# Performance work log

Measured on AMD Instinct MI355X. Metric: run time of the kernel, lower is better.

The kernel has to match this reference:

```python
import jax, jax.numpy as jnp
import numpy as np

H = 128; B = 128; NA = 32; N = B * NA; NH = 4; DH = H // NH; F = 2 * H + 3


def _ln(x, g, b, eps=1e-5):
    m = x.mean(-1, keepdims=True)
    v = ((x - m) ** 2).mean(-1, keepdims=True)
    return (x - m) / jnp.sqrt(v + eps) * g + b


def _silu(x):
    return x * jax.nn.sigmoid(x)


def setup_inputs() -> dict:
    key = jax.random.key(0)
    ks = jax.random.split(key, 16)
    def rn(i, shape, s=0.05):
        return jax.random.normal(ks[i], shape, jnp.float32) * s
    return dict(
        num_atoms=jnp.full((B,), NA, dtype=jnp.int32),
        elems=jax.random.randint(ks[0], (N,), 0, 119),
        cell=jnp.tile(10.0 * jnp.eye(3, dtype=jnp.float32), (B, 1)),  # [3B,3]
        coord=jax.random.uniform(ks[1], (N, 3), jnp.float32, 1.0, 9.0),
        emb=rn(2, (119, H), 1.0),
        ln_in_g=jnp.ones((H,), jnp.float32), ln_in_b=jnp.zeros((H,), jnp.float32),
        attn_in_w=rn(3, (H, 3 * H)), attn_in_b=jnp.zeros((3 * H,), jnp.float32),
        attn_out_w=rn(4, (H, H)), attn_out_b=jnp.zeros((H,), jnp.float32),
        ce_w1=rn(5, (3, H)), ce_b1=jnp.zeros((H,), jnp.float32),
        ce_w2=rn(6, (H, H)), ce_b2=jnp.zeros((H,), jnp.float32),
        ln_feat_g=jnp.ones((F,), jnp.float32), ln_feat_b=jnp.zeros((F,), jnp.float32),
        op_w1=rn(7, (F, H)), op_b1=jnp.zeros((H,), jnp.float32),
        op_ln1_g=jnp.ones((H,), jnp.float32), op_ln1_b=jnp.zeros((H,), jnp.float32),
        res_w1=rn(8, (H, H)), res_b1=jnp.zeros((H,), jnp.float32),
        res_ln_g=jnp.ones((H,), jnp.float32), res_ln_b=jnp.zeros((H,), jnp.float32),
        res_w2=rn(9, (H, H)), res_b2=jnp.zeros((H,), jnp.float32),
        op_ln2_g=jnp.ones((H,), jnp.float32), op_ln2_b=jnp.zeros((H,), jnp.float32),
        op_w3=rn(10, (H, 3)), op_b3=jnp.zeros((3,), jnp.float32),
    )


def reference(num_atoms, elems, cell, coord, emb, ln_in_g, ln_in_b,
              attn_in_w, attn_in_b, attn_out_w, attn_out_b,
              ce_w1, ce_b1, ce_w2, ce_b2, ln_feat_g, ln_feat_b,
              op_w1, op_b1, op_ln1_g, op_ln1_b,
              res_w1, res_b1, res_ln_g, res_ln_b, res_w2, res_b2,
              op_ln2_g, op_ln2_b, op_w3, op_b3):
    n = coord.shape[0]
    # atom embedding + input LayerNorm
    x = _ln(emb[elems], ln_in_g, ln_in_b)
    # unbatched multihead self-attention over all atoms (seq_len = n)
    qkv = x @ attn_in_w + attn_in_b
    q, k, v = jnp.split(qkv, 3, axis=-1)
    q = q.reshape(n, NH, DH); k = k.reshape(n, NH, DH); v = v.reshape(n, NH, DH)
    a = jax.nn.softmax(jnp.einsum('qhd,khd->hqk', q, k) / np.float32(np.sqrt(DH)), axis=-1)
    x = jnp.einsum('hqk,khd->qhd', a, v).reshape(n, H) @ attn_out_w + attn_out_b
    # cell encoder on [3B,3] rows
    cf = _silu(cell @ ce_w1 + ce_b1) @ ce_w2 + ce_b2
    bidx = jnp.repeat(jnp.arange(num_atoms.shape[0]), num_atoms, total_repeat_length=n)
    # torch: cf.repeat(B,1)[batch_idx] == cf[batch_idx] since batch_idx < B
    comb = _ln(jnp.concatenate([x, cf[bidx], coord], axis=-1), ln_feat_g, ln_feat_b)
    # offset predictor
    h = _silu(_ln(comb @ op_w1 + op_b1, op_ln1_g, op_ln1_b))
    h = h + (_silu(_ln(h @ res_w1 + res_b1, res_ln_g, res_ln_b)) @ res_w2 + res_b2)
    h = _ln(h, op_ln2_g, op_ln2_b)
    offset = jnp.tanh(h @ op_w3 + op_b3) * 0.01
    perturbed = coord + offset
    # per-molecule clamp: segment gather of per-cell-row min/max replaces the python loop
    c3 = cell.reshape(-1, 3, 3)           # [B,3,3]
    cmin = c3.min(axis=2) + 1e-6          # [B,3]
    cmax = c3.max(axis=2) - 1e-6          # [B,3]
    return jnp.clip(perturbed, cmin[bidx], cmax[bidx])
```

## Files before the change

kernel.cpp:

```cpp
#include <hip/hip_runtime.h>
#include <hip/hip_bf16.h>
#include <math.h>
#include <stdint.h>

#define NATOMS 4096
#define HD     128
#define NHEAD  4
#define DHEAD  32
#define FDIM   259
#define BATCH  128
#define H3X    384
#define SPLIT  4

typedef __attribute__((ext_vector_type(8))) short short8;
typedef __attribute__((ext_vector_type(4))) float float4v;
typedef __attribute__((ext_vector_type(16))) float f32x16;

__device__ __forceinline__ ushort f2bf(float f) {
    uint32_t u = __float_as_uint(f);
    return (ushort)((u + 0x7fffu + ((u >> 16) & 1u)) >> 16);
}
__device__ __forceinline__ float b2f(ushort u) {
    return __uint_as_float(((uint32_t)u) << 16);
}
__device__ __forceinline__ f32x16 z16() {
    f32x16 v;
#pragma unroll
    for (int i = 0; i < 16; i++) v[i] = 0.f;
    return v;
}

__global__ __launch_bounds__(256) void k_qkv(const int* __restrict__ elems,
                                             const float* __restrict__ emb,
                                             const float* __restrict__ lg,
                                             const float* __restrict__ lb,
                                             const float* __restrict__ qkvw,
                                             const float* __restrict__ bias,
                                             ushort* __restrict__ Qb, ushort* __restrict__ Kb,
                                             ushort* __restrict__ VTb2) {
    __shared__ alignas(16) ushort Wl[48 * 512];
    __shared__ alignas(16) ushort Af[4][64][8];
    __shared__ alignas(16) ushort vt[128][16];
    const int t = threadIdx.x, w = t >> 6, lane = t & 63, quad = lane >> 4, lq = lane & 15;
    const int rg = blockIdx.x >> 1, half = blockIdx.x & 1;
    const int rb = rg * 16;

#pragma unroll
    for (int m = 0; m < 12; m++) {
        int s = t + 256 * m;
        int chunk = s >> 6, l = s & 63;
        int ntl = chunk >> 2, kt = chunk & 3;
        int q8 = (l >> 4) * 8, lqq = l & 15;
        int n = half * 192 + ntl * 16 + lqq;
        int k0 = kt * 32 + q8;
        ushort o[8];
#pragma unroll
        for (int j = 0; j < 8; j++) o[j] = f2bf(qkvw[(k0 + j) * H3X + n]);
        *(uint4*)&Wl[(chunk << 9) + (l << 3)] = *(uint4*)o;
    }

    {
        int row = t >> 4, seg = t & 15;
        int e = elems[rb + row];
        const float* ep = emb + (size_t)e * HD + seg * 8;
        float v[8]; float s = 0.f, ss = 0.f;
#pragma unroll
        for (int j = 0; j < 8; j++) { v[j] = ep[j]; s += v[j]; ss += v[j] * v[j]; }
#pragma unroll
        for (int m = 1; m < 16; m <<= 1) { s += __shfl_xor(s, m); ss += __shfl_xor(ss, m); }
        float mean = s * (1.f / HD);
        float inv = rsqrtf(ss * (1.f / HD) - mean * mean + 1e-5f);
        ushort o[8];
#pragma unroll
        for (int j = 0; j < 8; j++)
            o[j] = f2bf((v[j] - mean) * inv * lg[seg * 8 + j] + lb[seg * 8 + j]);
        *(uint4*)&Af[seg >> 2][(seg & 3) * 16 + row][0] = *(uint4*)o;
    }
    __syncthreads();

    float4v acc[3];
#pragma unroll
    for (int i = 0; i < 3; i++) acc[i] = (float4v){0.f, 0.f, 0.f, 0.f};
#pragma unroll
    for (int kt = 0; kt < 4; kt++) {
        short8 af = *(const short8*)&Af[kt][lane][0];
#pragma unroll
        for (int i = 0; i < 3; i++) {
            short8 wf = *(const short8*)&Wl[((((w * 3 + i) << 2) + kt) << 9) + (lane << 3)];
            acc[i] = __builtin_amdgcn_mfma_f32_16x16x32_bf16(af, wf, acc[i], 0, 0, 0);
        }
    }
#pragma unroll
    for (int i = 0; i < 3; i++) {
        int col = lq + 16 * (half * 12 + w * 3 + i);
        float bb = bias[col];
#pragma unroll
        for (int r = 0; r < 4; r++) {
            float c = acc[i][r] + bb;
            int rowin = quad * 4 + r;
            int row = rb + rowin;
            if (col < 128) {
                Qb[(size_t)(((col >> 5) * NATOMS) + row) * 32 + (col & 31)] = f2bf(c * 0.25503483f);
            } else if (col < 256) {
                int cc = col - 128;
                Kb[(size_t)(((cc >> 5) * NATOMS) + row) * 32 + (cc & 31)] = f2bf(c);
            } else {
                vt[col - 256][rowin] = f2bf(c);
            }
        }
    }
    __syncthreads();
    if (half == 1 && t < 128) {
        int hh = t >> 5, d = t & 31;
        uint4 a0 = *(const uint4*)&vt[t][0];
        uint4 a1 = *(const uint4*)&vt[t][8];
        ushort* dst = VTb2 + ((size_t)(hh * 64 + (rb >> 6)) * 32 + d) * 64 + (rb & 63);
        *(uint4*)(dst) = a0;
        *(uint4*)(dst + 8) = a1;
    }
}

__global__ __launch_bounds__(256) void k_attn(const ushort* __restrict__ Qb,
                                              const ushort* __restrict__ Kb,
                                              const ushort* __restrict__ VTb2,
                                              ushort* __restrict__ Opart,
                                              float* __restrict__ lpart,
                                              const int* __restrict__ num_atoms,
                                              const float* __restrict__ cell,
                                              const float* __restrict__ aow,
                                              const float* __restrict__ op1w,
                                              const float* __restrict__ r1w,
                                              const float* __restrict__ r2w,
                                              const float* __restrict__ ce_w1,
                                              const float* __restrict__ ce_b1,
                                              const float* __restrict__ ce_w2,
                                              const float* __restrict__ ce_b2,
                                              int* __restrict__ bidx,
                                              float* __restrict__ cmin,
                                              float* __restrict__ cmax,
                                              ushort* __restrict__ Wao,
                                              ushort* __restrict__ Wop1,
                                              ushort* __restrict__ Wr1,
                                              ushort* __restrict__ Wr2,
                                              float* __restrict__ CF) {
    __shared__ alignas(16) ushort P_s[4][32 * 72];
    __shared__ alignas(16) float OL[2][32 * 36];
    __shared__ float LL[2][32];
    const int t = threadIdx.x;

    if (blockIdx.z == SPLIT) {
        float* hs = (float*)&P_s[0][0];
        int* start = (int*)&P_s[1][0];
        const int mid = blockIdx.y * 64 + blockIdx.x;
        for (int j = mid * 256 + t; j < 86016; j += 65536) {
            if (j < 16384) {
                int k = j >> 7, n = j & 127;
                Wao[n * 128 + k] = f2bf(aow[j]);
            } else if (j < 49536) {
                int jj = j - 16384; int k = jj >> 7, n = jj & 127;
                Wop1[n * 288 + k] = f2bf(op1w[jj]);
            } else if (j < 53248) {
                int jj = j - 49536; int n = jj & 127, k = 259 + (jj >> 7);
                Wop1[n * 288 + k] = 0;
            } else if (j < 69632) {
                int jj = j - 53248; int k = jj >> 7, n = jj & 127;
                Wr1[n * 128 + k] = f2bf(r1w[jj]);
            } else {
                int jj = j - 69632; int k = jj >> 7, n = jj & 127;
                Wr2[n * 128 + k] = f2bf(r2w[jj]);
            }
        }
        if (mid < 128) {
            if (t < 128) {
                float c0 = cell[mid * 3 + 0], c1 = cell[mid * 3 + 1], c2 = cell[mid * 3 + 2];
                float h = c0 * ce_w1[t] + c1 * ce_w1[HD + t] + c2 * ce_w1[2 * HD + t] + ce_b1[t];
                h = h / (1.f + __expf(-h));
                hs[t] = h;
            }
            __syncthreads();
            if (t < 128) {
                float acc = ce_b2[t];
#pragma unroll 8
                for (int k = 0; k < HD; k++) acc += hs[k] * ce_w2[k * HD + t];
                CF[mid * HD + t] = acc;
            }
        } else if (mid == 128) {
            if (t == 0) {
                int pos = 0;
                for (int b = 0; b < BATCH; b++) { start[b] = pos; pos += num_atoms[b]; }
                start[BATCH] = pos;
            }
            __syncthreads();
            if (t < 128) {
                int s = min(start[t], NATOMS), e = min(start[t + 1], NATOMS);
                for (int j = s; j < e; j++) bidx[j] = t;
                if (t == 0) {
                    int total = min(start[BATCH], NATOMS);
                    for (int j = total; j < NATOMS; j++) bidx[j] = BATCH - 1;
                }
            }
            for (int rr = t; rr < BATCH * 3; rr += 256) {
                float a0 = cell[rr * 3 + 0], a1 = cell[rr * 3 + 1], a2 = cell[rr * 3 + 2];
                cmin[rr] = fminf(a0, fminf(a1, a2)) + 1e-6f;
                cmax[rr] = fmaxf(a0, fmaxf(a1, a2)) - 1e-6f;
            }
        }
        return;
    }

    const int w = t >> 6, lane = t & 63;
    const int l31 = lane & 31, hi = lane >> 5;
    const int qt = w & 1, kh2 = w >> 1;
    const int h = blockIdx.y, sp = blockIdx.z;
    const int q0 = blockIdx.x * 64;
    const int qrow = q0 + qt * 32 + l31;

    short8 qf0 = *(const short8*)(Qb + (size_t)(h * NATOMS + qrow) * 32 + hi * 8);
    short8 qf1 = *(const short8*)(Qb + (size_t)(h * NATOMS + qrow) * 32 + 16 + hi * 8);
    f32x16 O = z16();
    float lp = 0.f;
    ushort* Pw = &P_s[w][0];
    const int kstart = sp * (NATOMS / SPLIT) + kh2 * 64;

    for (int ck = 0; ck < (NATOMS / SPLIT) / 128; ck++) {
        int kb = kstart + ck * 128;
        const ushort* vbase = VTb2 + ((size_t)(h * 64 + (kb >> 6)) * 32 + l31) * 64;
#pragma unroll
        for (int kt = 0; kt < 2; kt++) {
            int kk = kb + kt * 32;
            const ushort* kp = Kb + (size_t)(h * NATOMS + kk + l31) * 32 + hi * 8;
            short8 kf0 = *(const short8*)(kp);
            short8 kf1 = *(const short8*)(kp + 16);
            f32x16 S = z16();
            __builtin_amdgcn_s_setprio(1);
            S = __builtin_amdgcn_mfma_f32_32x32x16_bf16(kf0, qf0, S, 0, 0, 0);
            S = __builtin_amdgcn_mfma_f32_32x32x16_bf16(kf1, qf1, S, 0, 0, 0);
            __builtin_amdgcn_s_setprio(0);
#pragma unroll
            for (int c = 0; c < 4; c++) {
                float p0 = exp2f(S[4 * c + 0]);
                float p1 = exp2f(S[4 * c + 1]);
                float p2 = exp2f(S[4 * c + 2]);
                float p3 = exp2f(S[4 * c + 3]);
                lp += (p0 + p1) + (p2 + p3);
                uint2 u;
                asm("v_cvt_pk_bf16_f32 %0, %1, %2" : "=v"(u.x) : "v"(p0), "v"(p1));
                asm("v_cvt_pk_bf16_f32 %0, %1, %2" : "=v"(u.y) : "v"(p2), "v"(p3));
                *(uint2*)(&Pw[l31 * 72 + kt * 32 + c * 8 + hi * 4]) = u;
            }
#pragma unroll
            for (int wd = 0; wd < 2; wd++) {
                int koff = kt * 32 + wd * 16;
                short8 vf = *(const short8*)(vbase + koff + hi * 8);
                short8 pf = *(const short8*)(&Pw[l31 * 72 + koff + hi * 8]);
                __builtin_amdgcn_s_setprio(1);
                O = __builtin_amdgcn_mfma_f32_32x32x16_bf16(vf, pf, O, 0, 0, 0);
                __builtin_amdgcn_s_setprio(0);
            }
        }
    }
    lp += __shfl_xor(lp, 32);
    if (kh2 == 0) {
#pragma unroll
        for (int c = 0; c < 4; c++) {
            float4 f = {O[4 * c + 0], O[4 * c + 1], O[4 * c + 2], O[4 * c + 3]};
            *(float4*)(&OL[qt][l31 * 36 + c * 8 + hi * 4]) = f;
        }
        if (hi == 0) LL[qt][l31] = lp;
    }
    __syncthreads();
    if (kh2 == 1) {
        lp += LL[qt][l31];
#pragma unroll
        for (int c = 0; c < 4; c++) {
            float4 f = *(const float4*)(&OL[qt][l31 * 36 + c * 8 + hi * 4]);
            float o0 = O[4 * c + 0] + f.x, o1 = O[4 * c + 1] + f.y;
            float o2 = O[4 * c + 2] + f.z, o3 = O[4 * c + 3] + f.w;
            uint2 u;
            u.x = (uint32_t)f2bf(o0) | ((uint32_t)f2bf(o1) << 16);
            u.y = (uint32_t)f2bf(o2) | ((uint32_t)f2bf(o3) << 16);
            *(uint2*)(Opart + (size_t)(sp * NATOMS + qrow) * HD + h * 32 + c * 8 + hi * 4) = u;
        }
        if (hi == 0) lpart[sp * (NHEAD * NATOMS) + h * NATOMS + qrow] = lp;
    }
}

__global__ __launch_bounds__(512) void k_back(
        const ushort* __restrict__ Opart, const float* __restrict__ lpart,
        const ushort* __restrict__ Wao, const float* __restrict__ aob,
        const float* __restrict__ CF, const float* __restrict__ coord,
        const int* __restrict__ bidx,
        const float* __restrict__ fg, const float* __restrict__ fb,
        const ushort* __restrict__ Wop1, const float* __restrict__ op1b,
        const float* __restrict__ l1g, const float* __restrict__ l1b,
        const ushort* __restrict__ Wr1, const float* __restrict__ r1b,
        const float* __restrict__ rlg, const float* __restrict__ rlb,
        const ushort* __restrict__ Wr2, const float* __restrict__ r2b,
        const float* __restrict__ l2g, const float* __restrict__ l2b,
        const float* __restrict__ w3, const float* __restrict__ b3,
        const float* __restrict__ cmin, const float* __restrict__ cmax,
        float* __restrict__ out) {
    __shared__ alignas(16) ushort AF1[9][64][8];
    __shared__ alignas(16) ushort AF2[4][64][8];
    __shared__ alignas(16) ushort AF3[4][64][8];
    __shared__ float RED[8][16][4];
    __shared__ float REDC[16][2];
    __shared__ float COORDS[16][3];
    const int t = threadIdx.x, w = t >> 6, lane = t & 63, quad = lane >> 4, lq = lane & 15;
    const int rb = blockIdx.x * 16;
    const int col = lq + 16 * w;

    const int arow = rb + lq;
    float4v a0 = {0.f, 0.f, 0.f, 0.f};
#pragma unroll
    for (int h = 0; h < 4; h++) {
        float l = 0.f;
#pragma unroll
        for (int s = 0; s < SPLIT; s++) l += lpart[s * (NHEAD * NATOMS) + h * NATOMS + arow];
        float inv = 1.f / l;
        float pv[8];
#pragma unroll
        for (int j = 0; j < 8; j++) pv[j] = 0.f;
#pragma unroll
        for (int s = 0; s < SPLIT; s++) {
            short8 ov = *(const short8*)(Opart + (size_t)(s * NATOMS + arow) * HD + h * 32 + quad * 8);
#pragma unroll
            for (int j = 0; j < 8; j++) pv[j] += b2f((ushort)ov[j]);
        }
        short8 af;
#pragma unroll
        for (int j = 0; j < 8; j++) af[j] = (short)f2bf(pv[j] * inv);
        short8 w0 = *(const short8*)(Wao + (size_t)col * HD + h * 32 + quad * 8);
        a0 = __builtin_amdgcn_mfma_f32_16x16x32_bf16(af, w0, a0, 0, 0, 0);
    }
    float x1[4];
#pragma unroll
    for (int r = 0; r < 4; r++) x1[r] = a0[r] + aob[col];

    float cfv[4];
#pragma unroll
    for (int r = 0; r < 4; r++) cfv[r] = CF[bidx[rb + quad * 4 + r] * HD + col];
#pragma unroll
    for (int r = 0; r < 4; r++) {
        float s1 = x1[r] + cfv[r];
        float s2 = x1[r] * x1[r] + cfv[r] * cfv[r];
#pragma unroll
        for (int m = 1; m < 16; m <<= 1) { s1 += __shfl_xor(s1, m); s2 += __shfl_xor(s2, m); }
        if (lq == 0) { RED[w][quad * 4 + r][0] = s1; RED[w][quad * 4 + r][1] = s2; }
    }
    if (t < 16) {
        float c0 = coord[(rb + t) * 3 + 0], c1 = coord[(rb + t) * 3 + 1], c2 = coord[(rb + t) * 3 + 2];
        COORDS[t][0] = c0; COORDS[t][1] = c1; COORDS[t][2] = c2;
        REDC[t][0] = c0 + c1 + c2; REDC[t][1] = c0 * c0 + c1 * c1 + c2 * c2;
    }
    if (t < 64) { uint4 z = {0, 0, 0, 0}; *(uint4*)&AF1[8][t][0] = z; }
    __syncthreads();
#pragma unroll
    for (int r = 0; r < 4; r++) {
        int ri = quad * 4 + r;
        float s1 = REDC[ri][0], s2 = REDC[ri][1];
#pragma unroll
        for (int ww = 0; ww < 8; ww++) { s1 += RED[ww][ri][0]; s2 += RED[ww][ri][1]; }
        float mn = s1 * (1.f / FDIM);
        float iv = rsqrtf(s2 * (1.f / FDIM) - mn * mn + 1e-5f);
        float vx = (x1[r] - mn) * iv * fg[col] + fb[col];
        float vc = (cfv[r] - mn) * iv * fg[col + 128] + fb[col + 128];
        AF1[col >> 5][((col >> 3) & 3) * 16 + ri][col & 7] = f2bf(vx);
        int c2 = col + 128;
        AF1[c2 >> 5][((c2 >> 3) & 3) * 16 + ri][c2 & 7] = f2bf(vc);
    }
    if (t < 16) {
        float s1 = REDC[t][0], s2 = REDC[t][1];
#pragma unroll
        for (int ww = 0; ww < 8; ww++) { s1 += RED[ww][t][0]; s2 += RED[ww][t][1]; }
        float mn = s1 * (1.f / FDIM);
        float iv = rsqrtf(s2 * (1.f / FDIM) - mn * mn + 1e-5f);
#pragma unroll
        for (int c = 0; c < 3; c++)
            AF1[8][t][c] = f2bf((COORDS[t][c] - mn) * iv * fg[256 + c] + fb[256 + c]);
    }
    __syncthreads();

    float4v cv = {0.f, 0.f, 0.f, 0.f};
#pragma unroll
    for (int kt = 0; kt < 9; kt++) {
        short8 af = *(const short8*)&AF1[kt][lane][0];
        short8 w0 = *(const short8*)(Wop1 + (size_t)col * 288 + kt * 32 + quad * 8);
        cv = __builtin_amdgcn_mfma_f32_16x16x32_bf16(af, w0, cv, 0, 0, 0);
    }
    float h0[4];
#pragma unroll
    for (int r = 0; r < 4; r++) {
        h0[r] = cv[r] + op1b[col];
        float s1 = h0[r], s2 = h0[r] * h0[r];
#pragma unroll
        for (int m = 1; m < 16; m <<= 1) { s1 += __shfl_xor(s1, m); s2 += __shfl_xor(s2, m); }
        if (lq == 0) { RED[w][quad * 4 + r][0] = s1; RED[w][quad * 4 + r][1] = s2; }
    }
    __syncthreads();
#pragma unroll
    for (int r = 0; r < 4; r++) {
        int ri = quad * 4 + r;
        float s1 = 0.f, s2 = 0.f;
#pragma unroll
        for (int ww = 0; ww < 8; ww++) { s1 += RED[ww][ri][0]; s2 += RED[ww][ri][1]; }
        float mn = s1 * (1.f / HD);
        float iv = rsqrtf(s2 * (1.f / HD) - mn * mn + 1e-5f);
        float o = (h0[r] - mn) * iv * l1g[col] + l1b[col];
        o = o / (1.f + __expf(-o));
        AF2[col >> 5][((col >> 3) & 3) * 16 + ri][col & 7] = f2bf(o);
    }
    __syncthreads();

    float4v dv = {0.f, 0.f, 0.f, 0.f};
#pragma unroll
    for (int kt = 0; kt < 4; kt++) {
        short8 af = *(const short8*)&AF2[kt][lane][0];
        short8 w0 = *(const short8*)(Wr1 + (size_t)col * HD + kt * 32 + quad * 8);
        dv = __builtin_amdgcn_mfma_f32_16x16x32_bf16(af, w0, dv, 0, 0, 0);
    }
    float e0[4];
#pragma unroll
    for (int r = 0; r < 4; r++) {
        e0[r] = dv[r] + r1b[col];
        float s1 = e0[r], s2 = e0[r] * e0[r];
#pragma unroll
        for (int m = 1; m < 16; m <<= 1) { s1 += __shfl_xor(s1, m); s2 += __shfl_xor(s2, m); }
        if (lq == 0) { RED[w][quad * 4 + r][0] = s1; RED[w][quad * 4 + r][1] = s2; }
    }
    __syncthreads();
#pragma unroll
    for (int r = 0; r < 4; r++) {
        int ri = quad * 4 + r;
        float s1 = 0.f, s2 = 0.f;
#pragma unroll
        for (int ww = 0; ww < 8; ww++) { s1 += RED[ww][ri][0]; s2 += RED[ww][ri][1]; }
        float mn = s1 * (1.f / HD);
        float iv = rsqrtf(s2 * (1.f / HD) - mn * mn + 1e-5f);
        float o = (e0[r] - mn) * iv * rlg[col] + rlb[col];
        o = o / (1.f + __expf(-o));
        AF3[col >> 5][((col >> 3) & 3) * 16 + ri][col & 7] = f2bf(o);
    }
    __syncthreads();

    float4v fv = {0.f, 0.f, 0.f, 0.f};
#pragma unroll
    for (int kt = 0; kt < 4; kt++) {
        short8 af = *(const short8*)&AF3[kt][lane][0];
        short8 w0 = *(const short8*)(Wr2 + (size_t)col * HD + kt * 32 + quad * 8);
        fv = __builtin_amdgcn_mfma_f32_16x16x32_bf16(af, w0, fv, 0, 0, 0);
    }
    float g0r[4];
#pragma unroll
    for (int r = 0; r < 4; r++) {
        int ri = quad * 4 + r;
        float rs = b2f(AF2[col >> 5][((col >> 3) & 3) * 16 + ri][col & 7]);
        g0r[r] = fv[r] + r2b[col] + rs;
        float s1 = g0r[r], s2 = g0r[r] * g0r[r];
#pragma unroll
        for (int m = 1; m < 16; m <<= 1) { s1 += __shfl_xor(s1, m); s2 += __shfl_xor(s2, m); }
        if (lq == 0) { RED[w][ri][0] = s1; RED[w][ri][1] = s2; }
    }
    __syncthreads();
    float tp[4][3];
#pragma unroll
    for (int r = 0; r < 4; r++) {
        int ri = quad * 4 + r;
        float s1 = 0.f, s2 = 0.f;
#pragma unroll
        for (int ww = 0; ww < 8; ww++) { s1 += RED[ww][ri][0]; s2 += RED[ww][ri][1]; }
        float mn = s1 * (1.f / HD);
        float iv = rsqrtf(s2 * (1.f / HD) - mn * mn + 1e-5f);
        float h2 = (g0r[r] - mn) * iv * l2g[col] + l2b[col];
#pragma unroll
        for (int c = 0; c < 3; c++) {
            float v = h2 * w3[col * 3 + c];
#pragma unroll
            for (int m = 1; m < 16; m <<= 1) v += __shfl_xor(v, m);
            tp[r][c] = v;
        }
    }
    __syncthreads();
    if (lq == 0) {
#pragma unroll
        for (int r = 0; r < 4; r++) {
            RED[w][quad * 4 + r][0] = tp[r][0];
            RED[w][quad * 4 + r][1] = tp[r][1];
            RED[w][quad * 4 + r][2] = tp[r][2];
        }
    }
    __syncthreads();
    if (t < 16) {
        int bi = bidx[rb + t];
#pragma unroll
        for (int c = 0; c < 3; c++) {
            float sv = 0.f;
#pragma unroll
            for (int ww = 0; ww < 8; ww++) sv += RED[ww][t][c];
            float off = tanhf(sv + b3[c]) * 0.01f;
            float pert = COORDS[t][c] + off;
            pert = fminf(fmaxf(pert, cmin[bi * 3 + c]), cmax[bi * 3 + c]);
            out[(rb + t) * 3 + c] = pert;
        }
    }
}

extern "C" void kernel_launch(void* const* d_in, const int* in_sizes, int n_in,
                              void* d_out, int out_size, void* d_ws, size_t ws_size,
                              hipStream_t stream) {
    const int* num_atoms = (const int*)d_in[0];
    const int* elems = (const int*)d_in[1];
    const float* cell = (const float*)d_in[2];
    const float* coord = (const float*)d_in[3];
    const float* emb = (const float*)d_in[4];
    const float* ln_in_g = (const float*)d_in[5];
    const float* ln_in_b = (const float*)d_in[6];
    const float* attn_in_w = (const float*)d_in[7];
    const float* attn_in_b = (const float*)d_in[8];
    const float* attn_out_w = (const float*)d_in[9];
    const float* attn_out_b = (const float*)d_in[10];
    const float* ce_w1 = (const float*)d_in[11];
    const float* ce_b1 = (const float*)d_in[12];
    const float* ce_w2 = (const float*)d_in[13];
    const float* ce_b2 = (const float*)d_in[14];
    const float* ln_feat_g = (const float*)d_in[15];
    const float* ln_feat_b = (const float*)d_in[16];
    const float* op_w1 = (const float*)d_in[17];
    const float* op_b1 = (const float*)d_in[18];
    const float* op_ln1_g = (const float*)d_in[19];
    const float* op_ln1_b = (const float*)d_in[20];
    const float* res_w1 = (const float*)d_in[21];
    const float* res_b1 = (const float*)d_in[22];
    const float* res_ln_g = (const float*)d_in[23];
    const float* res_ln_b = (const float*)d_in[24];
    const float* res_w2 = (const float*)d_in[25];
    const float* res_b2 = (const float*)d_in[26];
    const float* op_ln2_g = (const float*)d_in[27];
    const float* op_ln2_b = (const float*)d_in[28];
    const float* op_w3 = (const float*)d_in[29];
    const float* op_b3 = (const float*)d_in[30];

    char* ws = (char*)d_ws;
    const size_t MB = 1u << 20;
    ushort* Qb = (ushort*)(ws);
    ushort* Kb = (ushort*)(ws + 1 * MB);
    ushort* VTb2 = (ushort*)(ws + 2 * MB);
    ushort* Opart = (ushort*)(ws + 3 * MB);
    float* lpart = (float*)(ws + 7 * MB);
    int* bidx = (int*)(ws + 7 * MB + (256u << 10));
    float* cmin = (float*)(ws + 7 * MB + (272u << 10));
    float* cmax = (float*)(ws + 7 * MB + (274u << 10));
    float* CF = (float*)(ws + 7 * MB + (276u << 10));
    ushort* Wao = (ushort*)(ws + 7 * MB + (436u << 10));
    ushort* Wop1 = (ushort*)(ws + 7 * MB + (468u << 10));
    ushort* Wr1 = (ushort*)(ws + 7 * MB + (540u << 10));
    ushort* Wr2 = (ushort*)(ws + 7 * MB + (572u << 10));

    k_qkv<<<512, 256, 0, stream>>>(elems, emb, ln_in_g, ln_in_b, attn_in_w, attn_in_b,
                                   Qb, Kb, VTb2);
    k_attn<<<dim3(NATOMS / 64, NHEAD, SPLIT + 1), 256, 0, stream>>>(
        Qb, Kb, VTb2, Opart, lpart,
        num_atoms, cell, attn_out_w, op_w1, res_w1, res_w2,
        ce_w1, ce_b1, ce_w2, ce_b2, bidx, cmin, cmax,
        Wao, Wop1, Wr1, Wr2, CF);
    k_back<<<256, 512, 0, stream>>>(Opart, lpart, Wao, attn_out_b, CF, coord, bidx,
                                    ln_feat_g, ln_feat_b, Wop1, op_b1, op_ln1_g, op_ln1_b,
                                    Wr1, res_b1, res_ln_g, res_ln_b, Wr2, res_b2,
                                    op_ln2_g, op_ln2_b, op_w3, op_b3, cmin, cmax,
                                    (float*)d_out);
}
```

Measured before the change: 172.1 us.

## Fuse three kernels into one persistent kernel with software grid barriers

Merges the QKV projection, split-K attention, and back-end MLP kernels into a single 512-block kernel. The phases are separated by atomic-counter grid barriers and share LDS through a union. QKV weight fragments now go straight into registers instead of being staged in LDS. The aim is to remove kernel launch gaps and tail effects between stages. The cost is a memset, spin-wait barriers that assume all 512 blocks are co-resident, and possibly higher register pressure at 512 threads.

```diff
diff --git a/kernel.cpp b/kernel.cpp
--- a/kernel.cpp
+++ b/kernel.cpp
@@ -30,477 +30,483 @@
     return v;
 }
 
-__global__ __launch_bounds__(256) void k_qkv(const int* __restrict__ elems,
-                                             const float* __restrict__ emb,
-                                             const float* __restrict__ lg,
-                                             const float* __restrict__ lb,
-                                             const float* __restrict__ qkvw,
-                                             const float* __restrict__ bias,
-                                             ushort* __restrict__ Qb, ushort* __restrict__ Kb,
-                                             ushort* __restrict__ VTb2) {
-    __shared__ alignas(16) ushort Wl[48 * 512];
-    __shared__ alignas(16) ushort Af[4][64][8];
-    __shared__ alignas(16) ushort vt[128][16];
-    const int t = threadIdx.x, w = t >> 6, lane = t & 63, quad = lane >> 4, lq = lane & 15;
-    const int rg = blockIdx.x >> 1, half = blockIdx.x & 1;
-    const int rb = rg * 16;
-
-#pragma unroll
-    for (int m = 0; m < 12; m++) {
-        int s = t + 256 * m;
-        int chunk = s >> 6, l = s & 63;
-        int ntl = chunk >> 2, kt = chunk & 3;
-        int q8 = (l >> 4) * 8, lqq = l & 15;
-        int n = half * 192 + ntl * 16 + lqq;
-        int k0 = kt * 32 + q8;
-        ushort o[8];
-#pragma unroll
-        for (int j = 0; j < 8; j++) o[j] = f2bf(qkvw[(k0 + j) * H3X + n]);
-        *(uint4*)&Wl[(chunk << 9) + (l << 3)] = *(uint4*)o;
-    }
-
-    {
-        int row = t >> 4, seg = t & 15;
-        int e = elems[rb + row];
-        const float* ep = emb + (size_t)e * HD + seg * 8;
-        float v[8]; float s = 0.f, ss = 0.f;
-#pragma unroll
-        for (int j = 0; j < 8; j++) { v[j] = ep[j]; s += v[j]; ss += v[j] * v[j]; }
-#pragma unroll
-        for (int m = 1; m < 16; m <<= 1) { s += __shfl_xor(s, m); ss += __shfl_xor(ss, m); }
-        float mean = s * (1.f / HD);
-        float inv = rsqrtf(ss * (1.f / HD) - mean * mean + 1e-5f);
-        ushort o[8];
-#pragma unroll
-        for (int j = 0; j < 8; j++)
-            o[j] = f2bf((v[j] - mean) * inv * lg[seg * 8 + j] + lb[seg * 8 + j]);
-        *(uint4*)&Af[seg >> 2][(seg & 3) * 16 + row][0] = *(uint4*)o;
+__device__ __forceinline__ void gbar(uint* cnt, uint target) {
+    __syncthreads();
+    if (threadIdx.x == 0) {
+        __threadfence();
+        atomicAdd(cnt, 1u);
+        while (__hip_atomic_load(cnt, __ATOMIC_RELAXED, __HIP_MEMORY_SCOPE_AGENT) < target)
+            __builtin_amdgcn_s_sleep(2);
     }
     __syncthreads();
-
-    float4v acc[3];
-#pragma unroll
-    for (int i = 0; i < 3; i++) acc[i] = (float4v){0.f, 0.f, 0.f, 0.f};
-#pragma unroll
-    for (int kt = 0; kt < 4; kt++) {
-        short8 af = *(const short8*)&Af[kt][lane][0];
-#pragma unroll
-        for (int i = 0; i < 3; i++) {
-            short8 wf = *(const short8*)&Wl[((((w * 3 + i) << 2) + kt) << 9) + (lane << 3)];
-            acc[i] = __builtin_amdgcn_mfma_f32_16x16x32_bf16(af, wf, acc[i], 0, 0, 0);
-        }
-    }
-#pragma unroll
-    for (int i = 0; i < 3; i++) {
-        int col = lq + 16 * (half * 12 + w * 3 + i);
-        float bb = bias[col];
-#pragma unroll
-        for (int r = 0; r < 4; r++) {
-            float c = acc[i][r] + bb;
-            int rowin = quad * 4 + r;
-            int row = rb + rowin;
-            if (col < 128) {
-                Qb[(size_t)(((col >> 5) * NATOMS) + row) * 32 + (col & 31)] = f2bf(c * 0.25503483f);
-            } else if (col < 256) {
-                int cc = col - 128;
-                Kb[(size_t)(((cc >> 5) * NATOMS) + row) * 32 + (cc & 31)] = f2bf(c);
-            } else {
-                vt[col - 256][rowin] = f2bf(c);
-            }
-        }
-    }
-    __syncthreads();
-    if (half == 1 && t < 128) {
-        int hh = t >> 5, d = t & 31;
-        uint4 a0 = *(const uint4*)&vt[t][0];
-        uint4 a1 = *(const uint4*)&vt[t][8];
-        ushort* dst = VTb2 + ((size_t)(hh * 64 + (rb >> 6)) * 32 + d) * 64 + (rb & 63);
-        *(uint4*)(dst) = a0;
-        *(uint4*)(dst + 8) = a1;
-    }
+    __threadfence();
 }
 
-__global__ __launch_bounds__(256) void k_attn(const ushort* __restrict__ Qb,
-                                              const ushort* __restrict__ Kb,
-                                              const ushort* __restrict__ VTb2,
-                                              ushort* __restrict__ Opart,
-                                              float* __restrict__ lpart,
-                                              const int* __restrict__ num_atoms,
-                                              const float* __restrict__ cell,
-                                              const float* __restrict__ aow,
-                                              const float* __restrict__ op1w,
-                                              const float* __restrict__ r1w,
-                                              const float* __restrict__ r2w,
-                                              const float* __restrict__ ce_w1,
-                                              const float* __restrict__ ce_b1,
-                                              const float* __restrict__ ce_w2,
-                                              const float* __restrict__ ce_b2,
-                                              int* __restrict__ bidx,
-                                              float* __restrict__ cmin,
-                                              float* __restrict__ cmax,
-                                              ushort* __restrict__ Wao,
-                                              ushort* __restrict__ Wop1,
-                                              ushort* __restrict__ Wr1,
-                                              ushort* __restrict__ Wr2,
-                                              float* __restrict__ CF) {
-    __shared__ alignas(16) ushort P_s[4][32 * 72];
-    __shared__ alignas(16) float OL[2][32 * 36];
-    __shared__ float LL[2][32];
-    const int t = threadIdx.x;
-
-    if (blockIdx.z == SPLIT) {
-        float* hs = (float*)&P_s[0][0];
-        int* start = (int*)&P_s[1][0];
-        const int mid = blockIdx.y * 64 + blockIdx.x;
-        for (int j = mid * 256 + t; j < 86016; j += 65536) {
-            if (j < 16384) {
-                int k = j >> 7, n = j & 127;
-                Wao[n * 128 + k] = f2bf(aow[j]);
-            } else if (j < 49536) {
-                int jj = j - 16384; int k = jj >> 7, n = jj & 127;
-                Wop1[n * 288 + k] = f2bf(op1w[jj]);
-            } else if (j < 53248) {
-                int jj = j - 49536; int n = jj & 127, k = 259 + (jj >> 7);
-                Wop1[n * 288 + k] = 0;
-            } else if (j < 69632) {
-                int jj = j - 53248; int k = jj >> 7, n = jj & 127;
-                Wr1[n * 128 + k] = f2bf(r1w[jj]);
-            } else {
-                int jj = j - 69632; int k = jj >> 7, n = jj & 127;
-                Wr2[n * 128 + k] = f2bf(r2w[jj]);
-            }
-        }
-        if (mid < 128) {
-            if (t < 128) {
-                float c0 = cell[mid * 3 + 0], c1 = cell[mid * 3 + 1], c2 = cell[mid * 3 + 2];
-                float h = c0 * ce_w1[t] + c1 * ce_w1[HD + t] + c2 * ce_w1[2 * HD + t] + ce_b1[t];
-                h = h / (1.f + __expf(-h));
-                hs[t] = h;
-            }
-            __syncthreads();
-            if (t < 128) {
-                float acc = ce_b2[t];
-#pragma unroll 8
-                for (int k = 0; k < HD; k++) acc += hs[k] * ce_w2[k * HD + t];
-                CF[mid * HD + t] = acc;
-            }
-        } else if (mid == 128) {
-            if (t == 0) {
-                int pos = 0;
-                for (int b = 0; b < BATCH; b++) { start[b] = pos; pos += num_atoms[b]; }
-                start[BATCH] = pos;
-            }
-            __syncthreads();
-            if (t < 128) {
-                int s = min(start[t], NATOMS), e = min(start[t + 1], NATOMS);
-                for (int j = s; j < e; j++) bidx[j] = t;
-                if (t == 0) {
-                    int total = min(start[BATCH], NATOMS);
-                    for (int j = total; j < NATOMS; j++) bidx[j] = BATCH - 1;
-                }
-            }
-            for (int rr = t; rr < BATCH * 3; rr += 256) {
-                float a0 = cell[rr * 3 + 0], a1 = cell[rr * 3 + 1], a2 = cell[rr * 3 + 2];
-                cmin[rr] = fminf(a0, fminf(a1, a2)) + 1e-6f;
-                cmax[rr] = fmaxf(a0, fmaxf(a1, a2)) - 1e-6f;
-            }
-        }
-        return;
-    }
-
-    const int w = t >> 6, lane = t & 63;
-    const int l31 = lane & 31, hi = lane >> 5;
-    const int qt = w & 1, kh2 = w >> 1;
-    const int h = blockIdx.y, sp = blockIdx.z;
-    const int q0 = blockIdx.x * 64;
-    const int qrow = q0 + qt * 32 + l31;
-
-    short8 qf0 = *(const short8*)(Qb + (size_t)(h * NATOMS + qrow) * 32 + hi * 8);
-    short8 qf1 = *(const short8*)(Qb + (size_t)(h * NATOMS + qrow) * 32 + 16 + hi * 8);
-    f32x16 O = z16();
-    float lp = 0.f;
-    ushort* Pw = &P_s[w][0];
-    const int kstart = sp * (NATOMS / SPLIT) + kh2 * 64;
-
-    for (int ck = 0; ck < (NATOMS / SPLIT) / 128; ck++) {
-        int kb = kstart + ck * 128;
-        const ushort* vbase = VTb2 + ((size_t)(h * 64 + (kb >> 6)) * 32 + l31) * 64;
-#pragma unroll
-        for (int kt = 0; kt < 2; kt++) {
-            int kk = kb + kt * 32;
-            const ushort* kp = Kb + (size_t)(h * NATOMS + kk + l31) * 32 + hi * 8;
-            short8 kf0 = *(const short8*)(kp);
-            short8 kf1 = *(const short8*)(kp + 16);
-            f32x16 S = z16();
-            __builtin_amdgcn_s_setprio(1);
-            S = __builtin_amdgcn_mfma_f32_32x32x16_bf16(kf0, qf0, S, 0, 0, 0);
-            S = __builtin_amdgcn_mfma_f32_32x32x16_bf16(kf1, qf1, S, 0, 0, 0);
-            __builtin_amdgcn_s_setprio(0);
-#pragma unroll
-            for (int c = 0; c < 4; c++) {
-                float p0 = exp2f(S[4 * c + 0]);
-                float p1 = exp2f(S[4 * c + 1]);
-                float p2 = exp2f(S[4 * c + 2]);
-                float p3 = exp2f(S[4 * c + 3]);
-                lp += (p0 + p1) + (p2 + p3);
-                uint2 u;
-                asm("v_cvt_pk_bf16_f32 %0, %1, %2" : "=v"(u.x) : "v"(p0), "v"(p1));
-                asm("v_cvt_pk_bf16_f32 %0, %1, %2" : "=v"(u.y) : "v"(p2), "v"(p3));
-                *(uint2*)(&Pw[l31 * 72 + kt * 32 + c * 8 + hi * 4]) = u;
-            }
-#pragma unroll
-            for (int wd = 0; wd < 2; wd++) {
-                int koff = kt * 32 + wd * 16;
-                short8 vf = *(const short8*)(vbase + koff + hi * 8);
-                short8 pf = *(const short8*)(&Pw[l31 * 72 + koff + hi * 8]);
-                __builtin_amdgcn_s_setprio(1);
-                O = __builtin_amdgcn_mfma_f32_32x32x16_bf16(vf, pf, O, 0, 0, 0);
-                __builtin_amdgcn_s_setprio(0);
-            }
-        }
-    }
-    lp += __shfl_xor(lp, 32);
-    if (kh2 == 0) {
-#pragma unroll
-        for (int c = 0; c < 4; c++) {
-            float4 f = {O[4 * c + 0], O[4 * c + 1], O[4 * c + 2], O[4 * c + 3]};
-            *(float4*)(&OL[qt][l31 * 36 + c * 8 + hi * 4]) = f;
-        }
-        if (hi == 0) LL[qt][l31] = lp;
-    }
-    __syncthreads();
-    if (kh2 == 1) {
-        lp += LL[qt][l31];
-#pragma unroll
-        for (int c = 0; c < 4; c++) {
-            float4 f = *(const float4*)(&OL[qt][l31 * 36 + c * 8 + hi * 4]);
-            float o0 = O[4 * c + 0] + f.x, o1 = O[4 * c + 1] + f.y;
-            float o2 = O[4 * c + 2] + f.z, o3 = O[4 * c + 3] + f.w;
-            uint2 u;
-            u.x = (uint32_t)f2bf(o0) | ((uint32_t)f2bf(o1) << 16);
-            u.y = (uint32_t)f2bf(o2) | ((uint32_t)f2bf(o3) << 16);
-            *(uint2*)(Opart + (size_t)(sp * NATOMS + qrow) * HD + h * 32 + c * 8 + hi * 4) = u;
-        }
-        if (hi == 0) lpart[sp * (NHEAD * NATOMS) + h * NATOMS + qrow] = lp;
-    }
-}
-
-__global__ __launch_bounds__(512) void k_back(
-        const ushort* __restrict__ Opart, const float* __restrict__ lpart,
-        const ushort* __restrict__ Wao, const float* __restrict__ aob,
-        const float* __restrict__ CF, const float* __restrict__ coord,
-        const int* __restrict__ bidx,
+struct LdsQ {
+    alignas(16) ushort Af[4][64][8];
+    alignas(16) ushort vt[128][16];
+};
+struct LdsA {
+    alignas(16) ushort P[2][4][2304];
+    alignas(16) float OL[2][2][1152];
+    float LL[2][2][32];
+    float hs[2][128];
+    int start[2][132];
+};
+struct LdsB {
+    alignas(16) ushort AF1[9][64][8];
+    alignas(16) ushort AF2[4][64][8];
+    alignas(16) ushort AF3[4][64][8];
+    float RED[8][16][4];
+    float REDC[16][2];
+    float COORDS[16][3];
+};
+union LdsU { LdsQ q; LdsA a; LdsB bk; };
+
+__global__ __launch_bounds__(512, 4) void k_fused(
+        const int* __restrict__ elems, const float* __restrict__ emb,
+        const float* __restrict__ lgi, const float* __restrict__ lbi,
+        const float* __restrict__ qkvw, const float* __restrict__ qkvb,
+        ushort* __restrict__ Qb, ushort* __restrict__ Kb, ushort* __restrict__ VTb2,
+        ushort* __restrict__ Opart, float* __restrict__ lpart,
+        const int* __restrict__ num_atoms, const float* __restrict__ cell,
+        const float* __restrict__ aow, const float* __restrict__ op1w,
+        const float* __restrict__ r1w, const float* __restrict__ r2w,
+        const float* __restrict__ ce_w1, const float* __restrict__ ce_b1,
+        const float* __restrict__ ce_w2, const float* __restrict__ ce_b2,
+        int* __restrict__ bidx, float* __restrict__ cmin, float* __restrict__ cmax,
+        ushort* __restrict__ Wao, ushort* __restrict__ Wop1,
+        ushort* __restrict__ Wr1, ushort* __restrict__ Wr2, float* __restrict__ CF,
+        const float* __restrict__ aob, const float* __restrict__ coord,
         const float* __restrict__ fg, const float* __restrict__ fb,
-        const ushort* __restrict__ Wop1, const float* __restrict__ op1b,
+        const float* __restrict__ op1b,
         const float* __restrict__ l1g, const float* __restrict__ l1b,
-        const ushort* __restrict__ Wr1, const float* __restrict__ r1b,
-        const float* __restrict__ rlg, const float* __restrict__ rlb,
-        const ushort* __restrict__ Wr2, const float* __restrict__ r2b,
+        const float* __restrict__ r1b, const float* __restrict__ rlg,
+        const float* __restrict__ rlb, const float* __restrict__ r2b,
         const float* __restrict__ l2g, const float* __restrict__ l2b,
         const float* __restrict__ w3, const float* __restrict__ b3,
-        const float* __restrict__ cmin, const float* __restrict__ cmax,
-        float* __restrict__ out) {
-    __shared__ alignas(16) ushort AF1[9][64][8];
-    __shared__ alignas(16) ushort AF2[4][64][8];
-    __shared__ alignas(16) ushort AF3[4][64][8];
-    __shared__ float RED[8][16][4];
-    __shared__ float REDC[16][2];
-    __shared__ float COORDS[16][3];
-    const int t = threadIdx.x, w = t >> 6, lane = t & 63, quad = lane >> 4, lq = lane & 15;
-    const int rb = blockIdx.x * 16;
-    const int col = lq + 16 * w;
-
-    const int arow = rb + lq;
-    float4v a0 = {0.f, 0.f, 0.f, 0.f};
-#pragma unroll
-    for (int h = 0; h < 4; h++) {
-        float l = 0.f;
-#pragma unroll
-        for (int s = 0; s < SPLIT; s++) l += lpart[s * (NHEAD * NATOMS) + h * NATOMS + arow];
-        float inv = 1.f / l;
-        float pv[8];
-#pragma unroll
-        for (int j = 0; j < 8; j++) pv[j] = 0.f;
-#pragma unroll
-        for (int s = 0; s < SPLIT; s++) {
-            short8 ov = *(const short8*)(Opart + (size_t)(s * NATOMS + arow) * HD + h * 32 + quad * 8);
-#pragma unroll
-            for (int j = 0; j < 8; j++) pv[j] += b2f((ushort)ov[j]);
-        }
-        short8 af;
-#pragma unroll
-        for (int j = 0; j < 8; j++) af[j] = (short)f2bf(pv[j] * inv);
-        short8 w0 = *(const short8*)(Wao + (size_t)col * HD + h * 32 + quad * 8);
-        a0 = __builtin_amdgcn_mfma_f32_16x16x32_bf16(af, w0, a0, 0, 0, 0);
+        uint* __restrict__ bar, float* __restrict__ out) {
+    __shared__ LdsU u;
+    const int t512 = threadIdx.x;
+    const int b = blockIdx.x;
+
+    {
+        const int rg = b >> 1, qh = b & 1, rb = rg * 16;
+        const int w = t512 >> 6, lane = t512 & 63, quad = lane >> 4, lq = lane & 15;
+        const bool act = t512 < 256;
+        short8 wfrag[12];
+        if (act) {
+#pragma unroll
+            for (int kt = 0; kt < 4; kt++)
+#pragma unroll
+                for (int i = 0; i < 3; i++) {
+                    int n = qh * 192 + (w * 3 + i) * 16 + lq;
+                    int k0 = kt * 32 + quad * 8;
+                    ushort o[8];
+#pragma unroll
+                    for (int j = 0; j < 8; j++) o[j] = f2bf(qkvw[(size_t)(k0 + j) * H3X + n]);
+                    wfrag[kt * 3 + i] = *(const short8*)o;
+                }
+            int row = t512 >> 4, seg = t512 & 15;
+            int e = elems[rb + row];
+            const float* ep = emb + (size_t)e * HD + seg * 8;
+            float v[8]; float s = 0.f, ss = 0.f;
+#pragma unroll
+            for (int j = 0; j < 8; j++) { v[j] = ep[j]; s += v[j]; ss += v[j] * v[j]; }
+#pragma unroll
+            for (int m = 1; m < 16; m <<= 1) { s += __shfl_xor(s, m); ss += __shfl_xor(ss, m); }
+            float mean = s * (1.f / HD);
+            float inv = rsqrtf(ss * (1.f / HD) - mean * mean + 1e-5f);
+            ushort o[8];
+#pragma unroll
+            for (int j = 0; j < 8; j++)
+                o[j] = f2bf((v[j] - mean) * inv * lgi[seg * 8 + j] + lbi[seg * 8 + j]);
+            *(uint4*)&u.q.Af[seg >> 2][(seg & 3) * 16 + row][0] = *(uint4*)o;
+        }
+        __syncthreads();
+        if (act) {
+            float4v acc[3];
+#pragma unroll
+            for (int i = 0; i < 3; i++) acc[i] = (float4v){0.f, 0.f, 0.f, 0.f};
+#pragma unroll
+            for (int kt = 0; kt < 4; kt++) {
+                short8 af = *(const short8*)&u.q.Af[kt][lane][0];
+#pragma unroll
+                for (int i = 0; i < 3; i++)
+                    acc[i] = __builtin_amdgcn_mfma_f32_16x16x32_bf16(af, wfrag[kt * 3 + i], acc[i], 0, 0, 0);
+            }
+#pragma unroll
+            for (int i = 0; i < 3; i++) {
+                int col = lq + 16 * (qh * 12 + w * 3 + i);
+                float bb = qkvb[col];
+#pragma unroll
+                for (int r = 0; r < 4; r++) {
+                    float c = acc[i][r] + bb;
+                    int rowin = quad * 4 + r;
+                    int row = rb + rowin;
+                    if (col < 128) {
+                        Qb[(size_t)(((col >> 5) * NATOMS) + row) * 32 + (col & 31)] = f2bf(c * 0.25503483f);
+                    } else if (col < 256) {
+                        int cc = col - 128;
+                        Kb[(size_t)(((cc >> 5) * NATOMS) + row) * 32 + (cc & 31)] = f2bf(c);
+                    } else {
+                        u.q.vt[col - 256][rowin] = f2bf(c);
+                    }
+                }
+            }
+        }
+        __syncthreads();
+        if (qh == 1 && t512 < 128) {
+            int hh = t512 >> 5, d = t512 & 31;
+            uint4 a0 = *(const uint4*)&u.q.vt[t512][0];
+            uint4 a1 = *(const uint4*)&u.q.vt[t512][8];
+            ushort* dst = VTb2 + ((size_t)(hh * 64 + (rb >> 6)) * 32 + d) * 64 + (rb & 63);
+            *(uint4*)(dst) = a0;
+            *(uint4*)(dst + 8) = a1;
+        }
     }
-    float x1[4];
-#pragma unroll
-    for (int r = 0; r < 4; r++) x1[r] = a0[r] + aob[col];
-
-    float cfv[4];
-#pragma unroll
-    for (int r = 0; r < 4; r++) cfv[r] = CF[bidx[rb + quad * 4 + r] * HD + col];
-#pragma unroll
-    for (int r = 0; r < 4; r++) {
-        float s1 = x1[r] + cfv[r];
-        float s2 = x1[r] * x1[r] + cfv[r] * cfv[r];
-#pragma unroll
-        for (int m = 1; m < 16; m <<= 1) { s1 += __shfl_xor(s1, m); s2 += __shfl_xor(s2, m); }
-        if (lq == 0) { RED[w][quad * 4 + r][0] = s1; RED[w][quad * 4 + r][1] = s2; }
+    gbar(bar, 512);
+
+    {
+        const int half = t512 >> 8, t = t512 & 255;
+        const int w = t >> 6, lane = t & 63;
+        const int slot = b * 2 + half;
+        for (int uu = slot; uu < 1280; uu += 1024) {
+            if (uu < 1024) {
+                const int qb_ = uu & 63, h = (uu >> 6) & 3, sp = uu >> 8;
+                const int l31 = lane & 31, hi = lane >> 5;
+                const int qt = w & 1, kh2 = w >> 1;
+                const int qrow = qb_ * 64 + qt * 32 + l31;
+
+                short8 qf0 = *(const short8*)(Qb + (size_t)(h * NATOMS + qrow) * 32 + hi * 8);
+                short8 qf1 = *(const short8*)(Qb + (size_t)(h * NATOMS + qrow) * 32 + 16 + hi * 8);
+                f32x16 O = z16();
+                float lp = 0.f;
+                ushort* Pw = &u.a.P[half][w][0];
+                const int kstart = sp * (NATOMS / SPLIT) + kh2 * 64;
+
+                for (int ck = 0; ck < (NATOMS / SPLIT) / 128; ck++) {
+                    int kb = kstart + ck * 128;
+                    const ushort* vbase = VTb2 + ((size_t)(h * 64 + (kb >> 6)) * 32 + l31) * 64;
+#pragma unroll
+                    for (int kt = 0; kt < 2; kt++) {
+                        int kk = kb + kt * 32;
+                        const ushort* kp = Kb + (size_t)(h * NATOMS + kk + l31) * 32 + hi * 8;
+                        short8 kf0 = *(const short8*)(kp);
+                        short8 kf1 = *(const short8*)(kp + 16);
+                        f32x16 S = z16();
+                        __builtin_amdgcn_s_setprio(1);
+                        S = __builtin_amdgcn_mfma_f32_32x32x16_bf16(kf0, qf0, S, 0, 0, 0);
+                        S = __builtin_amdgcn_mfma_f32_32x32x16_bf16(kf1, qf1, S, 0, 0, 0);
+                        __builtin_amdgcn_s_setprio(0);
+#pragma unroll
+                        for (int c = 0; c < 4; c++) {
+                            float p0 = exp2f(S[4 * c + 0]);
+                            float p1 = exp2f(S[4 * c + 1]);
+                            float p2 = exp2f(S[4 * c + 2]);
+                            float p3 = exp2f(S[4 * c + 3]);
+                            lp += (p0 + p1) + (p2 + p3);
+                            uint2 pk;
+                            asm("v_cvt_pk_bf16_f32 %0, %1, %2" : "=v"(pk.x) : "v"(p0), "v"(p1));
+                            asm("v_cvt_pk_bf16_f32 %0, %1, %2" : "=v"(pk.y) : "v"(p2), "v"(p3));
+                            *(uint2*)(&Pw[l31 * 72 + kt * 32 + c * 8 + hi * 4]) = pk;
+                        }
+#pragma unroll
+                        for (int wd = 0; wd < 2; wd++) {
+                            int koff = kt * 32 + wd * 16;
+                            short8 vf = *(const short8*)(vbase + koff + hi * 8);
+                            short8 pf = *(const short8*)(&Pw[l31 * 72 + koff + hi * 8]);
+                            __builtin_amdgcn_s_setprio(1);
+                            O = __builtin_amdgcn_mfma_f32_32x32x16_bf16(vf, pf, O, 0, 0, 0);
+                            __builtin_amdgcn_s_setprio(0);
+                        }
+                    }
+                }
+                lp += __shfl_xor(lp, 32);
+                if (kh2 == 0) {
+#pragma unroll
+                    for (int c = 0; c < 4; c++) {
+                        float4 f = {O[4 * c + 0], O[4 * c + 1], O[4 * c + 2], O[4 * c + 3]};
+                        *(float4*)(&u.a.OL[half][qt][l31 * 36 + c * 8 + hi * 4]) = f;
+                    }
+                    if (hi == 0) u.a.LL[half][qt][l31] = lp;
+                }
+                __syncthreads();
+                if (kh2 == 1) {
+                    lp += u.a.LL[half][qt][l31];
+#pragma unroll
+                    for (int c = 0; c < 4; c++) {
+                        float4 f = *(const float4*)(&u.a.OL[half][qt][l31 * 36 + c * 8 + hi * 4]);
+                        float o0 = O[4 * c + 0] + f.x, o1 = O[4 * c + 1] + f.y;
+                        float o2 = O[4 * c + 2] + f.z, o3 = O[4 * c + 3] + f.w;
+                        uint2 pk;
+                        pk.x = (uint32_t)f2bf(o0) | ((uint32_t)f2bf(o1) << 16);
+                        pk.y = (uint32_t)f2bf(o2) | ((uint32_t)f2bf(o3) << 16);
+                        *(uint2*)(Opart + (size_t)(sp * NATOMS + qrow) * HD + h * 32 + c * 8 + hi * 4) = pk;
+                    }
+                    if (hi == 0) lpart[sp * (NHEAD * NATOMS) + h * NATOMS + qrow] = lp;
+                }
+            } else {
+                const int mid = uu - 1024;
+                float* hs = u.a.hs[half];
+                int* start = u.a.start[half];
+                for (int j = mid * 256 + t; j < 86016; j += 65536) {
+                    if (j < 16384) {
+                        int k = j >> 7, n = j & 127;
+                        Wao[n * 128 + k] = f2bf(aow[j]);
+                    } else if (j < 49536) {
+                        int jj = j - 16384; int k = jj >> 7, n = jj & 127;
+                        Wop1[n * 288 + k] = f2bf(op1w[jj]);
+                    } else if (j < 53248) {
+                        int jj = j - 49536; int n = jj & 127, k = 259 + (jj >> 7);
+                        Wop1[n * 288 + k] = 0;
+                    } else if (j < 69632) {
+                        int jj = j - 53248; int k = jj >> 7, n = jj & 127;
+                        Wr1[n * 128 + k] = f2bf(r1w[jj]);
+                    } else {
+                        int jj = j - 69632; int k = jj >> 7, n = jj & 127;
+                        Wr2[n * 128 + k] = f2bf(r2w[jj]);
+                    }
+                }
+                if (mid < 128) {
+                    if (t < 128) {
+                        float c0 = cell[mid * 3 + 0], c1 = cell[mid * 3 + 1], c2 = cell[mid * 3 + 2];
+                        float h = c0 * ce_w1[t] + c1 * ce_w1[HD + t] + c2 * ce_w1[2 * HD + t] + ce_b1[t];
+                        h = h / (1.f + __expf(-h));
+                        hs[t] = h;
+                    }
+                } else if (mid == 128) {
+                    if (t == 0) {
+                        int pos = 0;
+                        for (int bb2 = 0; bb2 < BATCH; bb2++) { start[bb2] = pos; pos += num_atoms[bb2]; }
+                        start[BATCH] = pos;
+                    }
+                }
+                __syncthreads();
+                if (mid < 128) {
+                    if (t < 128) {
+                        float acc = ce_b2[t];
+#pragma unroll 8
+                        for (int k = 0; k < HD; k++) acc += hs[k] * ce_w2[k * HD + t];
+                        CF[mid * HD + t] = acc;
+                    }
+                } else if (mid == 128) {
+                    if (t < 128) {
+                        int s = min(start[t], NATOMS), e = min(start[t + 1], NATOMS);
+                        for (int j = s; j < e; j++) bidx[j] = t;
+                        if (t == 0) {
+                            int total = min(start[BATCH], NATOMS);
+                            for (int j = total; j < NATOMS; j++) bidx[j] = BATCH - 1;
+                        }
+                    }
+                    for (int rr = t; rr < BATCH * 3; rr += 256) {
+                        float a0 = cell[rr * 3 + 0], a1 = cell[rr * 3 + 1], a2 = cell[rr * 3 + 2];
+                        cmin[rr] = fminf(a0, fminf(a1, a2)) + 1e-6f;
+                        cmax[rr] = fmaxf(a0, fmaxf(a1, a2)) - 1e-6f;
+                    }
+                }
+            }
+        }
     }
-    if (t < 16) {
-        float c0 = coord[(rb + t) * 3 + 0], c1 = coord[(rb + t) * 3 + 1], c2 = coord[(rb + t) * 3 + 2];
-        COORDS[t][0] = c0; COORDS[t][1] = c1; COORDS[t][2] = c2;
-        REDC[t][0] = c0 + c1 + c2; REDC[t][1] = c0 * c0 + c1 * c1 + c2 * c2;
-    }
-    if (t < 64) { uint4 z = {0, 0, 0, 0}; *(uint4*)&AF1[8][t][0] = z; }
-    __syncthreads();
-#pragma unroll
-    for (int r = 0; r < 4; r++) {
-        int ri = quad * 4 + r;
-        float s1 = REDC[ri][0], s2 = REDC[ri][1];
-#pragma unroll
-        for (int ww = 0; ww < 8; ww++) { s1 += RED[ww][ri][0]; s2 += RED[ww][ri][1]; }
-        float mn = s1 * (1.f / FDIM);
-        float iv = rsqrtf(s2 * (1.f / FDIM) - mn * mn + 1e-5f);
-        float vx = (x1[r] - mn) * iv * fg[col] + fb[col];
-        float vc = (cfv[r] - mn) * iv * fg[col + 128] + fb[col + 128];
-        AF1[col >> 5][((col >> 3) & 3) * 16 + ri][col & 7] = f2bf(vx);
-        int c2 = col + 128;
-        AF1[c2 >> 5][((c2 >> 3) & 3) * 16 + ri][c2 & 7] = f2bf(vc);
-    }
-    if (t < 16) {
-        float s1 = REDC[t][0], s2 = REDC[t][1];
-#pragma unroll
-        for (int ww = 0; ww < 8; ww++) { s1 += RED[ww][t][0]; s2 += RED[ww][t][1]; }
-        float mn = s1 * (1.f / FDIM);
-        float iv = rsqrtf(s2 * (1.f / FDIM) - mn * mn + 1e-5f);
-#pragma unroll
-        for (int c = 0; c < 3; c++)
-            AF1[8][t][c] = f2bf((COORDS[t][c] - mn) * iv * fg[256 + c] + fb[256 + c]);
-    }
-    __syncthreads();
-
-    float4v cv = {0.f, 0.f, 0.f, 0.f};
-#pragma unroll
-    for (int kt = 0; kt < 9; kt++) {
-        short8 af = *(const short8*)&AF1[kt][lane][0];
-        short8 w0 = *(const short8*)(Wop1 + (size_t)col * 288 + kt * 32 + quad * 8);
-        cv = __builtin_amdgcn_mfma_f32_16x16x32_bf16(af, w0, cv, 0, 0, 0);
-    }
-    float h0[4];
-#pragma unroll
-    for (int r = 0; r < 4; r++) {
-        h0[r] = cv[r] + op1b[col];
-        float s1 = h0[r], s2 = h0[r] * h0[r];
-#pragma unroll
-        for (int m = 1; m < 16; m <<= 1) { s1 += __shfl_xor(s1, m); s2 += __shfl_xor(s2, m); }
-        if (lq == 0) { RED[w][quad * 4 + r][0] = s1; RED[w][quad * 4 + r][1] = s2; }
-    }
-    __syncthreads();
-#pragma unroll
-    for (int r = 0; r < 4; r++) {
-        int ri = quad * 4 + r;
-        float s1 = 0.f, s2 = 0.f;
-#pragma unroll
-        for (int ww = 0; ww < 8; ww++) { s1 += RED[ww][ri][0]; s2 += RED[ww][ri][1]; }
-        float mn = s1 * (1.f / HD);
-        float iv = rsqrtf(s2 * (1.f / HD) - mn * mn + 1e-5f);
-        float o = (h0[r] - mn) * iv * l1g[col] + l1b[col];
-        o = o / (1.f + __expf(-o));
-        AF2[col >> 5][((col >> 3) & 3) * 16 + ri][col & 7] = f2bf(o);
-    }
-    __syncthreads();
-
-    float4v dv = {0.f, 0.f, 0.f, 0.f};
-#pragma unroll
-    for (int kt = 0; kt < 4; kt++) {
-        short8 af = *(const short8*)&AF2[kt][lane][0];
-        short8 w0 = *(const short8*)(Wr1 + (size_t)col * HD + kt * 32 + quad * 8);
-        dv = __builtin_amdgcn_mfma_f32_16x16x32_bf16(af, w0, dv, 0, 0, 0);
-    }
-    float e0[4];
-#pragma unroll
-    for (int r = 0; r < 4; r++) {
-        e0[r] = dv[r] + r1b[col];
-        float s1 = e0[r], s2 = e0[r] * e0[r];
-#pragma unroll
-        for (int m = 1; m < 16; m <<= 1) { s1 += __shfl_xor(s1, m); s2 += __shfl_xor(s2, m); }
-        if (lq == 0) { RED[w][quad * 4 + r][0] = s1; RED[w][quad * 4 + r][1] = s2; }
-    }
-    __syncthreads();
-#pragma unroll
-    for (int r = 0; r < 4; r++) {
-        int ri = quad * 4 + r;
-        float s1 = 0.f, s2 = 0.f;
-#pragma unroll
-        for (int ww = 0; ww < 8; ww++) { s1 += RED[ww][ri][0]; s2 += RED[ww][ri][1]; }
-        float mn = s1 * (1.f / HD);
-        float iv = rsqrtf(s2 * (1.f / HD) - mn * mn + 1e-5f);
-        float o = (e0[r] - mn) * iv * rlg[col] + rlb[col];
-        o = o / (1.f + __expf(-o));
-        AF3[col >> 5][((col >> 3) & 3) * 16 + ri][col & 7] = f2bf(o);
-    }
-    __syncthreads();
-
-    float4v fv = {0.f, 0.f, 0.f, 0.f};
-#pragma unroll
-    for (int kt = 0; kt < 4; kt++) {
-        short8 af = *(const short8*)&AF3[kt][lane][0];
-        short8 w0 = *(const short8*)(Wr2 + (size_t)col * HD + kt * 32 + quad * 8);
-        fv = __builtin_amdgcn_mfma_f32_16x16x32_bf16(af, w0, fv, 0, 0, 0);
-    }
-    float g0r[4];
-#pragma unroll
-    for (int r = 0; r < 4; r++) {
-        int ri = quad * 4 + r;
-        float rs = b2f(AF2[col >> 5][((col >> 3) & 3) * 16 + ri][col & 7]);
-        g0r[r] = fv[r] + r2b[col] + rs;
-        float s1 = g0r[r], s2 = g0r[r] * g0r[r];
-#pragma unroll
-        for (int m = 1; m < 16; m <<= 1) { s1 += __shfl_xor(s1, m); s2 += __shfl_xor(s2, m); }
-        if (lq == 0) { RED[w][ri][0] = s1; RED[w][ri][1] = s2; }
-    }
-    __syncthreads();
-    float tp[4][3];
-#pragma unroll
-    for (int r = 0; r < 4; r++) {
-        int ri = quad * 4 + r;
-        float s1 = 0.f, s2 = 0.f;
-#pragma unroll
-        for (int ww = 0; ww < 8; ww++) { s1 += RED[ww][ri][0]; s2 += RED[ww][ri][1]; }
-        float mn = s1 * (1.f / HD);
-        float iv = rsqrtf(s2 * (1.f / HD) - mn * mn + 1e-5f);
-        float h2 = (g0r[r] - mn) * iv * l2g[col] + l2b[col];
-#pragma unroll
-        for (int c = 0; c < 3; c++) {
-            float v = h2 * w3[col * 3 + c];
-#pragma unroll
-            for (int m = 1; m < 16; m <<= 1) v += __shfl_xor(v, m);
-            tp[r][c] = v;
-        }
-    }
-    __syncthreads();
-    if (lq == 0) {
-#pragma unroll
-        for (int r = 0; r < 4; r++) {
-            RED[w][quad * 4 + r][0] = tp[r][0];
-            RED[w][quad * 4 + r][1] = tp[r][1];
-            RED[w][quad * 4 + r][2] = tp[r][2];
-        }
-    }
-    __syncthreads();
-    if (t < 16) {
-        int bi = bidx[rb + t];
-#pragma unroll
-        for (int c = 0; c < 3; c++) {
-            float sv = 0.f;
-#pragma unroll
-            for (int ww = 0; ww < 8; ww++) sv += RED[ww][t][c];
-            float off = tanhf(sv + b3[c]) * 0.01f;
-            float pert = COORDS[t][c] + off;
-            pert = fminf(fmaxf(pert, cmin[bi * 3 + c]), cmax[bi * 3 + c]);
-            out[(rb + t) * 3 + c] = pert;
+    gbar(bar, 1024);
+
+    if (b < 256) {
+        const int t = t512, w = t >> 6, lane = t & 63, quad = lane >> 4, lq = lane & 15;
+        const int rb = b * 16;
+        const int col = lq + 16 * w;
+
+        const int arow = rb + lq;
+        float4v a0 = {0.f, 0.f, 0.f, 0.f};
+#pragma unroll
+        for (int h = 0; h < 4; h++) {
+            float l = 0.f;
+#pragma unroll
+            for (int s = 0; s < SPLIT; s++) l += lpart[s * (NHEAD * NATOMS) + h * NATOMS + arow];
+            float inv = 1.f / l;
+            float pv[8];
+#pragma unroll
+            for (int j = 0; j < 8; j++) pv[j] = 0.f;
+#pragma unroll
+            for (int s = 0; s < SPLIT; s++) {
+                short8 ov = *(const short8*)(Opart + (size_t)(s * NATOMS + arow) * HD + h * 32 + quad * 8);
+#pragma unroll
+                for (int j = 0; j < 8; j++) pv[j] += b2f((ushort)ov[j]);
+            }
+            short8 af;
+#pragma unroll
+            for (int j = 0; j < 8; j++) af[j] = (short)f2bf(pv[j] * inv);
+            short8 w0 = *(const short8*)(Wao + (size_t)col * HD + h * 32 + quad * 8);
+            a0 = __builtin_amdgcn_mfma_f32_16x16x32_bf16(af, w0, a0, 0, 0, 0);
+        }
+        float x1[4];
+#pragma unroll
+        for (int r = 0; r < 4; r++) x1[r] = a0[r] + aob[col];
+
+        float cfv[4];
+#pragma unroll
+        for (int r = 0; r < 4; r++) cfv[r] = CF[bidx[rb + quad * 4 + r] * HD + col];
+#pragma unroll
+        for (int r = 0; r < 4; r++) {
+            float s1 = x1[r] + cfv[r];
+            float s2 = x1[r] * x1[r] + cfv[r] * cfv[r];
+#pragma unroll
+            for (int m = 1; m < 16; m <<= 1) { s1 += __shfl_xor(s1, m); s2 += __shfl_xor(s2, m); }
+            if (lq == 0) { u.bk.RED[w][quad * 4 + r][0] = s1; u.bk.RED[w][quad * 4 + r][1] = s2; }
+        }
+        if (t < 16) {
+            float c0 = coord[(rb + t) * 3 + 0], c1 = coord[(rb + t) * 3 + 1], c2 = coord[(rb + t) * 3 + 2];
+            u.bk.COORDS[t][0] = c0; u.bk.COORDS[t][1] = c1; u.bk.COORDS[t][2] = c2;
+            u.bk.REDC[t][0] = c0 + c1 + c2; u.bk.REDC[t][1] = c0 * c0 + c1 * c1 + c2 * c2;
+        }
+        if (t < 64) { uint4 z = {0, 0, 0, 0}; *(uint4*)&u.bk.AF1[8][t][0] = z; }
+        __syncthreads();
+#pragma unroll
+        for (int r = 0; r < 4; r++) {
+            int ri = quad * 4 + r;
+            float s1 = u.bk.REDC[ri][0], s2 = u.bk.REDC[ri][1];
+#pragma unroll
+            for (int ww = 0; ww < 8; ww++) { s1 += u.bk.RED[ww][ri][0]; s2 += u.bk.RED[ww][ri][1]; }
+            float mn = s1 * (1.f / FDIM);
+            float iv = rsqrtf(s2 * (1.f / FDIM) - mn * mn + 1e-5f);
+            float vx = (x1[r] - mn) * iv * fg[col] + fb[col];
+            float vc = (cfv[r] - mn) * iv * fg[col + 128] + fb[col + 128];
+            u.bk.AF1[col >> 5][((col >> 3) & 3) * 16 + ri][col & 7] = f2bf(vx);
+            int c2 = col + 128;
+            u.bk.AF1[c2 >> 5][((c2 >> 3) & 3) * 16 + ri][c2 & 7] = f2bf(vc);
+        }
+        if (t < 16) {
+            float s1 = u.bk.REDC[t][0], s2 = u.bk.REDC[t][1];
+#pragma unroll
+            for (int ww = 0; ww < 8; ww++) { s1 += u.bk.RED[ww][t][0]; s2 += u.bk.RED[ww][t][1]; }
+            float mn = s1 * (1.f / FDIM);
+            float iv = rsqrtf(s2 * (1.f / FDIM) - mn * mn + 1e-5f);
+#pragma unroll
+            for (int c = 0; c < 3; c++)
+                u.bk.AF1[8][t][c] = f2bf((u.bk.COORDS[t][c] - mn) * iv * fg[256 + c] + fb[256 + c]);
+        }
+        __syncthreads();
+
+        float4v cv = {0.f, 0.f, 0.f, 0.f};
+#pragma unroll
+        for (int kt = 0; kt < 9; kt++) {
+            short8 af = *(const short8*)&u.bk.AF1[kt][lane][0];
+            short8 w0 = *(const short8*)(Wop1 + (size_t)col * 288 + kt * 32 + quad * 8);
+            cv = __builtin_amdgcn_mfma_f32_16x16x32_bf16(af, w0, cv, 0, 0, 0);
+        }
+        float h0[4];
+#pragma unroll
+        for (int r = 0; r < 4; r++) {
+            h0[r] = cv[r] + op1b[col];
+            float s1 = h0[r], s2 = h0[r] * h0[r];
+#pragma unroll
+            for (int m = 1; m < 16; m <<= 1) { s1 += __shfl_xor(s1, m); s2 += __shfl_xor(s2, m); }
+            if (lq == 0) { u.bk.RED[w][quad * 4 + r][0] = s1; u.bk.RED[w][quad * 4 + r][1] = s2; }
+        }
+        __syncthreads();
+#pragma unroll
+        for (int r = 0; r < 4; r++) {
+            int ri = quad * 4 + r;
+            float s1 = 0.f, s2 = 0.f;
+#pragma unroll
+            for (int ww = 0; ww < 8; ww++) { s1 += u.bk.RED[ww][ri][0]; s2 += u.bk.RED[ww][ri][1]; }
+            float mn = s1 * (1.f / HD);
+            float iv = rsqrtf(s2 * (1.f / HD) - mn * mn + 1e-5f);
+            float o = (h0[r] - mn) * iv * l1g[col] + l1b[col];
+            o = o / (1.f + __expf(-o));
+            u.bk.AF2[col >> 5][((col >> 3) & 3) * 16 + ri][col & 7] = f2bf(o);
+        }
+        __syncthreads();
+
+        float4v dv = {0.f, 0.f, 0.f, 0.f};
+#pragma unroll
+        for (int kt = 0; kt < 4; kt++) {
+            short8 af = *(const short8*)&u.bk.AF2[kt][lane][0];
+            short8 w0 = *(const short8*)(Wr1 + (size_t)col * HD + kt * 32 + quad * 8);
+            dv = __builtin_amdgcn_mfma_f32_16x16x32_bf16(af, w0, dv, 0, 0, 0);
+        }
+        float e0[4];
+#pragma unroll
+        for (int r = 0; r < 4; r++) {
+            e0[r] = dv[r] + r1b[col];
+            float s1 = e0[r], s2 = e0[r] * e0[r];
+#pragma unroll
+            for (int m = 1; m < 16; m <<= 1) { s1 += __shfl_xor(s1, m); s2 += __shfl_xor(s2, m); }
+            if (lq == 0) { u.bk.RED[w][quad * 4 + r][0] = s1; u.bk.RED[w][quad * 4 + r][1] = s2; }
+        }
+        __syncthreads();
+#pragma unroll
+        for (int r = 0; r < 4; r++) {
+            int ri = quad * 4 + r;
+            float s1 = 0.f, s2 = 0.f;
+#pragma unroll
+            for (int ww = 0; ww < 8; ww++) { s1 += u.bk.RED[ww][ri][0]; s2 += u.bk.RED[ww][ri][1]; }
+            float mn = s1 * (1.f / HD);
+            float iv = rsqrtf(s2 * (1.f / HD) - mn * mn + 1e-5f);
+            float o = (e0[r] - mn) * iv * rlg[col] + rlb[col];
+            o = o / (1.f + __expf(-o));
+            u.bk.AF3[col >> 5][((col >> 3) & 3) * 16 + ri][col & 7] = f2bf(o);
+        }
+        __syncthreads();
+
+        float4v fv = {0.f, 0.f, 0.f, 0.f};
+#pragma unroll
+        for (int kt = 0; kt < 4; kt++) {
+            short8 af = *(const short8*)&u.bk.AF3[kt][lane][0];
+            short8 w0 = *(const short8*)(Wr2 + (size_t)col * HD + kt * 32 + quad * 8);
+            fv = __builtin_amdgcn_mfma_f32_16x16x32_bf16(af, w0, fv, 0, 0, 0);
+        }
+        float g0r[4];
+#pragma unroll
+        for (int r = 0; r < 4; r++) {
+            int ri = quad * 4 + r;
+            float rs = b2f(u.bk.AF2[col >> 5][((col >> 3) & 3) * 16 + ri][col & 7]);
+            g0r[r] = fv[r] + r2b[col] + rs;
+            float s1 = g0r[r], s2 = g0r[r] * g0r[r];
+#pragma unroll
+            for (int m = 1; m < 16; m <<= 1) { s1 += __shfl_xor(s1, m); s2 += __shfl_xor(s2, m); }
+            if (lq == 0) { u.bk.RED[w][ri][0] = s1; u.bk.RED[w][ri][1] = s2; }
+        }
+        __syncthreads();
+        float tp[4][3];
+#pragma unroll
+        for (int r = 0; r < 4; r++) {
+            int ri = quad * 4 + r;
+            float s1 = 0.f, s2 = 0.f;
+#pragma unroll
+            for (int ww = 0; ww < 8; ww++) { s1 += u.bk.RED[ww][ri][0]; s2 += u.bk.RED[ww][ri][1]; }
+            float mn = s1 * (1.f / HD);
+            float iv = rsqrtf(s2 * (1.f / HD) - mn * mn + 1e-5f);
+            float h2 = (g0r[r] - mn) * iv * l2g[col] + l2b[col];
+#pragma unroll
+            for (int c = 0; c < 3; c++) {
+                float v = h2 * w3[col * 3 + c];
+#pragma unroll
+                for (int m = 1; m < 16; m <<= 1) v += __shfl_xor(v, m);
+                tp[r][c] = v;
+            }
+        }
+        __syncthreads();
+        if (lq == 0) {
+#pragma unroll
+            for (int r = 0; r < 4; r++) {
+                u.bk.RED[w][quad * 4 + r][0] = tp[r][0];
+                u.bk.RED[w][quad * 4 + r][1] = tp[r][1];
+                u.bk.RED[w][quad * 4 + r][2] = tp[r][2];
+            }
+        }
+        __syncthreads();
+        if (t < 16) {
+            int bi = bidx[rb + t];
+#pragma unroll
+            for (int c = 0; c < 3; c++) {
+                float sv = 0.f;
+#pragma unroll
+                for (int ww = 0; ww < 8; ww++) sv += u.bk.RED[ww][t][c];
+                float off = tanhf(sv + b3[c]) * 0.01f;
+                float pert = u.bk.COORDS[t][c] + off;
+                pert = fminf(fmaxf(pert, cmin[bi * 3 + c]), cmax[bi * 3 + c]);
+                out[(rb + t) * 3 + c] = pert;
+            }
         }
     }
 }
@@ -555,17 +561,17 @@
     ushort* Wop1 = (ushort*)(ws + 7 * MB + (468u << 10));
     ushort* Wr1 = (ushort*)(ws + 7 * MB + (540u << 10));
     ushort* Wr2 = (ushort*)(ws + 7 * MB + (572u << 10));
-
-    k_qkv<<<512, 256, 0, stream>>>(elems, emb, ln_in_g, ln_in_b, attn_in_w, attn_in_b,
-                                   Qb, Kb, VTb2);
-    k_attn<<<dim3(NATOMS / 64, NHEAD, SPLIT + 1), 256, 0, stream>>>(
+    uint* bar = (uint*)(ws + 8 * MB);
+
+    hipMemsetAsync(bar, 0, 4, stream);
+    k_fused<<<512, 512, 0, stream>>>(
+        elems, emb, ln_in_g, ln_in_b, attn_in_w, attn_in_b,
         Qb, Kb, VTb2, Opart, lpart,
         num_atoms, cell, attn_out_w, op_w1, res_w1, res_w2,
-        ce_w1, ce_b1, ce_w2, ce_b2, bidx, cmin, cmax,
-        Wao, Wop1, Wr1, Wr2, CF);
-    k_back<<<256, 512, 0, stream>>>(Opart, lpart, Wao, attn_out_b, CF, coord, bidx,
-                                    ln_feat_g, ln_feat_b, Wop1, op_b1, op_ln1_g, op_ln1_b,
-                                    Wr1, res_b1, res_ln_g, res_ln_b, Wr2, res_b2,
-                                    op_ln2_g, op_ln2_b, op_w3, op_b3, cmin, cmax,
-                                    (float*)d_out);
+        ce_w1, ce_b1, ce_w2, ce_b2,
+        bidx, cmin, cmax, Wao, Wop1, Wr1, Wr2, CF,
+        attn_out_b, coord, ln_feat_g, ln_feat_b, op_b1,
+        op_ln1_g, op_ln1_b, res_b1, res_ln_g, res_ln_b, res_b2,
+        op_ln2_g, op_ln2_b, op_w3, op_b3,
+        bar, (float*)d_out);
 }
```

Result: slower. 391.8 us (+127.6%).
